# Performance work log

Hardware: AMD Instinct MI355X
Metric: run time of the kernel (lower is better)

Reference implementation:

```python
import jax, jax.numpy as jnp
import numpy as np
import math

B = 256        # batch
N = 262144     # n_data (memory bank size)
D = 128        # feat_dim
K = 4096       # number of negatives
MAX_NEGS = K   # K * max_hard_negatives_percentage (=1)
T = 0.07


def _l2norm(x):
    # Normalise(power=2): x / (sum(x^2, axis=1))^(1/2)
    return x / jnp.sqrt(jnp.sum(x * x, axis=1, keepdims=True))


def setup_inputs() -> dict:
    key = jax.random.key(0)
    k1, k2, k3, k4 = jax.random.split(key, 4)
    stdv = math.sqrt(3.0 / D)  # 1/sqrt(feat_dim/3)
    anchor_feature = _l2norm(jax.random.normal(k1, (B, D), dtype=jnp.float32))
    pair_feature = _l2norm(jax.random.normal(k2, (B, D), dtype=jnp.float32))
    memory_bank = jax.random.uniform(k3, (N, D), dtype=jnp.float32,
                                     minval=-stdv, maxval=stdv)
    membank_idx = jax.random.randint(k4, (B,), 0, N, dtype=jnp.int32)
    threshold = jnp.full((1,), 10.0, dtype=jnp.float32)  # no masking -> all-hard path
    return {"anchor_feature": anchor_feature, "pair_feature": pair_feature,
            "memory_bank": memory_bank, "membank_idx": membank_idx,
            "threshold": threshold}


def reference(anchor_feature, pair_feature, memory_bank, membank_idx, threshold):
    # ---- mine_negative_examples (no_grad in original) ----
    # NOTE: original does memory_bank.view(feat_dim, -1) == row-major reshape,
    # NOT a transpose. Replicate exactly.
    mem_r = memory_bank.reshape(D, N)                    # [D, N]
    scores = anchor_feature @ mem_r                      # [B, N]
    scores = jnp.where(scores >= threshold[0], jnp.float32(-2.0), scores)
    top_s, top_i = jax.lax.top_k(scores, K)              # [B, K]
    hard = jnp.minimum(jnp.sum(top_s != -2.0, axis=1), MAX_NEGS)  # [B]
    # random fill for positions beyond the hard count (uniform over bank;
    # original excludes a handful of indices via multinomial - negligible for large N)
    rand_i = jax.random.randint(jax.random.key(42), (B, K), 0, N, dtype=top_i.dtype)
    use_hard = jnp.arange(K)[None, :] < hard[:, None]    # [B, K]
    negatives = jnp.where(use_hard, top_i, rand_i)       # [B, K]

    # ---- contrast ----
    weight = jax.lax.stop_gradient(memory_bank[negatives])          # [B, K, D]
    weight = jnp.concatenate([pair_feature[:, None, :], weight], 1)  # slot 0 = positive, [B, K+1, D]
    out = jnp.exp(jnp.einsum('bkd,bd->bk', weight, anchor_feature) / T)  # [B, K+1]
    # params[2] == -1 initially -> Z_c = out.mean() * n_data (a detached scalar)
    Z = jax.lax.stop_gradient(jnp.mean(out) * N)
    return (out / Z)[:, :, None]                         # [B, K+1, 1]
```

## Files before the change

### kernel.cpp

```cpp
#include <hip/hip_runtime.h>
#include <math.h>

#define BB 256
#define NN 262144
#define DD 128
#define KK 4096
#define CAP 8192
#define NOUT (BB * (KK + 1))
#define THETA0 0.172f

#define RB 16
#define CB 1024
#define NRBLK (BB / RB)
#define NCSL (NN / CB)
#define SLOTS 56
#define PAD 32
#define SMEMS ((2 * 4 * CB) * 4 + RB * SLOTS * 8 + 3 * RB * 4)

typedef float f16v __attribute__((ext_vector_type(16)));

__global__ __launch_bounds__(256) void k_init(const float* __restrict__ anchor,
                                              float* __restrict__ At2,
                                              unsigned* __restrict__ cnt) {
  const int b = blockIdx.x;
  if (b < NRBLK) {
    for (int j = threadIdx.x; j < DD * 16; j += 256) {
      const int d = j >> 4, r = j & 15;
      At2[(size_t)b * DD * 16 + j] =
          anchor[(size_t)(b * RB + r) * DD + d];
    }
  } else {
    for (int i = threadIdx.x; i < BB * PAD; i += 256) cnt[i] = 0u;
  }
}

#define LOADA2(VA, VB, PTR, OFF0, OFF1)                                  \
  asm volatile("s_load_dwordx16 %0, %2, " OFF0 "\n\t"                    \
               "s_load_dwordx16 %1, %2, " OFF1 "\n\t"                    \
               "s_waitcnt lgkmcnt(0)"                                    \
               : "=&s"(VA), "=&s"(VB)                                    \
               : "s"(PTR));                                              \
  __builtin_amdgcn_sched_barrier(0);

__global__ __launch_bounds__(256, 4) void k_score(
    const float* __restrict__ bank, const float* __restrict__ At2,
    const float* __restrict__ thr, unsigned* __restrict__ cnt,
    unsigned long long* __restrict__ cand) {
  extern __shared__ float smem[];
  float* Bs = smem;
  unsigned long long* stash = (unsigned long long*)(smem + 2 * 4 * CB);
  unsigned* lcnt  = (unsigned*)(stash + RB * SLOTS);
  unsigned* lbase = lcnt + RB;
  unsigned* lm    = lbase + RB;

  const int tid = threadIdx.x;
  const int wave = tid >> 6;
  const int lane = tid & 63;
  const int bid = blockIdx.x;
  const int xcd = bid & 7;
  const int u = bid >> 3;
  const int rowblk = u & (NRBLK - 1);
  const int sgrp = u >> 4;
  const int rowbase = rowblk * RB;
  const int cb = (sgrp * 8 + xcd) * CB;

  const float* __restrict__ abase = At2 + (size_t)rowblk * DD * 16;

#define STAGE(SLOT, D0)                                                      \
  for (int t = wave; t < 16; t += 4) {                                       \
    const int d_ = t >> 2, q_ = t & 3;                                       \
    const float* gsrc =                                                      \
        bank + (size_t)((D0) + d_) * NN + cb + q_ * 256 + lane * 4;          \
    __builtin_amdgcn_global_load_lds(                                        \
        (const __attribute__((address_space(1))) void*)gsrc,                 \
        (__attribute__((address_space(3))) void*)                            \
            &Bs[((size_t)(SLOT)*4 + d_) * CB + q_ * 256],                    \
        16, 0, 0);                                                           \
  }

  STAGE(0, 0)
  STAGE(1, 4)

  const float tv = thr[0];

  float acc[64];
#pragma unroll
  for (int i = 0; i < 64; ++i) acc[i] = 0.f;

#define COMP_D(AV, DDI)                                                  \
  {                                                                      \
    const float4 bv = *(const float4*)&Bc[(DDI) * CB + 4 * tid];         \
    _Pragma("unroll") for (int r = 0; r < 16; ++r) {                     \
      acc[r * 4 + 0] = fmaf(AV[r], bv.x, acc[r * 4 + 0]);                \
      acc[r * 4 + 1] = fmaf(AV[r], bv.y, acc[r * 4 + 1]);                \
      acc[r * 4 + 2] = fmaf(AV[r], bv.z, acc[r * 4 + 2]);                \
      acc[r * 4 + 3] = fmaf(AV[r], bv.w, acc[r * 4 + 3]);                \
    }                                                                    \
  }

  for (int ch = 0; ch < 32; ++ch) {
    const float* __restrict__ Bc = &Bs[(size_t)(ch & 1) * 4 * CB];
    const float* pc = abase + ch * 64;

    if (ch < 31) { asm volatile("s_waitcnt vmcnt(4)" ::: "memory"); }
    else         { asm volatile("s_waitcnt vmcnt(0)" ::: "memory"); }
    __builtin_amdgcn_sched_barrier(0);

    f16v aA, aB, aC, aD;
    LOADA2(aA, aB, pc, "0x0", "0x40")
    COMP_D(aA, 0)
    COMP_D(aB, 1)
    LOADA2(aC, aD, pc, "0x80", "0xc0")
    COMP_D(aC, 2)
    COMP_D(aD, 3)

    if (ch < 30) {
      asm volatile("s_waitcnt lgkmcnt(0)" ::: "memory");
      __builtin_amdgcn_sched_barrier(0);
      STAGE(ch & 1, (ch + 2) * 4)
    }
  }
#undef COMP_D
#undef STAGE

  if (tid < RB) lcnt[tid] = 0u;
  __syncthreads();

#pragma unroll
  for (int r = 0; r < RB; ++r) {
#pragma unroll
    for (int c = 0; c < 4; ++c) {
      const float s = acc[r * 4 + c];
      if (s >= THETA0 && s < tv) {
        const unsigned col = (unsigned)(cb + tid * 4 + c);
        const unsigned long long key =
            ((unsigned long long)__float_as_uint(s) << 32) |
            (unsigned long long)(0xFFFFFFFFu - col);
        const unsigned lpos = atomicAdd(&lcnt[r], 1u);
        if (lpos < SLOTS) {
          stash[r * SLOTS + lpos] = key;
        } else {
          const unsigned gpos = atomicAdd(&cnt[(size_t)(rowbase + r) * PAD], 1u);
          if (gpos < CAP) cand[(size_t)(rowbase + r) * CAP + gpos] = key;
        }
      }
    }
  }
  __syncthreads();

  if (tid < RB) {
    const unsigned m = min(lcnt[tid], (unsigned)SLOTS);
    lm[tid] = m;
    lbase[tid] = atomicAdd(&cnt[(size_t)(rowbase + tid) * PAD], m);
  }
  __syncthreads();

  for (int i = tid; i < RB * SLOTS; i += 256) {
    const int r = i / SLOTS, j = i - r * SLOTS;
    if ((unsigned)j < lm[r]) {
      const unsigned pos = lbase[r] + (unsigned)j;
      if (pos < CAP) cand[(size_t)(rowbase + r) * CAP + pos] = stash[i];
    }
  }
}

__global__ void k_sort(const unsigned* __restrict__ cnt,
                       const unsigned long long* __restrict__ cand,
                       unsigned* __restrict__ neg) {
  extern __shared__ unsigned long long sk[];
  const int b = blockIdx.x;
  unsigned m = cnt[(size_t)b * PAD];
  if (m > CAP) m = CAP;

  for (int i = threadIdx.x; i < CAP; i += (int)blockDim.x)
    sk[i] = (i < (int)m) ? cand[(size_t)b * CAP + i] : 0ULL;
  __syncthreads();

  for (int k = 2; k <= CAP; k <<= 1) {
    for (int j = k >> 1; j > 0; j >>= 1) {
      for (int i = threadIdx.x; i < CAP / 2; i += (int)blockDim.x) {
        int t = i & (j - 1);
        int p = ((i - t) << 1) + t;
        int q = p + j;
        bool up = ((p & k) == 0);
        unsigned long long a = sk[p], c = sk[q];
        bool sw = up ? (a < c) : (a > c);
        if (sw) { sk[p] = c; sk[q] = a; }
      }
      __syncthreads();
    }
  }

  for (int i = threadIdx.x; i < KK; i += (int)blockDim.x) {
    unsigned idx = 0xFFFFFFFFu - (unsigned)(sk[i] & 0xFFFFFFFFull);
    neg[(size_t)b * KK + i] = (sk[i] == 0ULL) ? 0u : idx;
  }
}

__global__ __launch_bounds__(256) void k_contrast(
    const float* __restrict__ anchor, const float* __restrict__ pair,
    const float* __restrict__ bank, const unsigned* __restrict__ neg,
    float* __restrict__ out, double* __restrict__ zpart) {
  __shared__ __align__(16) float As[DD];
  __shared__ double wsum[4];
  const int bid = blockIdx.x;
  double myv;
  if (bid < BB * (KK / 256)) {
    const int b = bid >> 4;
    const int k = ((bid & 15) << 8) + threadIdx.x;
    if (threadIdx.x < DD) As[threadIdx.x] = anchor[(size_t)b * DD + threadIdx.x];
    __syncthreads();
    const unsigned idx = neg[(size_t)b * KK + k];
    const float4* __restrict__ rp = (const float4*)(bank + (size_t)idx * DD);
    const float4* __restrict__ apv = (const float4*)As;
    float s = 0.f;
#pragma unroll
    for (int q = 0; q < DD / 4; ++q) {
      float4 rv = rp[q], av = apv[q];
      s = fmaf(rv.x, av.x, s);
      s = fmaf(rv.y, av.y, s);
      s = fmaf(rv.z, av.z, s);
      s = fmaf(rv.w, av.w, s);
    }
    float e = expf(s * (1.0f / 0.07f));
    out[(size_t)b * (KK + 1) + 1 + k] = e;
    myv = (double)e;
  } else {
    const int b = threadIdx.x;
    const float* __restrict__ apr = anchor + (size_t)b * DD;
    const float* __restrict__ ppr = pair + (size_t)b * DD;
    float s = 0.f;
#pragma unroll
    for (int q = 0; q < DD; ++q) s = fmaf(apr[q], ppr[q], s);
    float e = expf(s * (1.0f / 0.07f));
    out[(size_t)b * (KK + 1)] = e;
    myv = (double)e;
  }
  for (int off = 32; off > 0; off >>= 1) myv += __shfl_down(myv, off, 64);
  if ((threadIdx.x & 63) == 0) wsum[threadIdx.x >> 6] = myv;
  __syncthreads();
  if (threadIdx.x == 0) zpart[bid] = (wsum[0] + wsum[1]) + (wsum[2] + wsum[3]);
}

__global__ void k_zreduce(const double* __restrict__ zpart, double* __restrict__ invZ) {
  __shared__ double w[16];
  double v = 0.0;
  for (int i = threadIdx.x; i < BB * (KK / 256) + 1; i += 1024) v += zpart[i];
  for (int off = 32; off > 0; off >>= 1) v += __shfl_down(v, off, 64);
  if ((threadIdx.x & 63) == 0) w[threadIdx.x >> 6] = v;
  __syncthreads();
  if (threadIdx.x == 0) {
    double t = 0.0;
    for (int q = 0; q < 16; ++q) t += w[q];
    double Z = t / ((double)BB * (double)(KK + 1)) * (double)NN;
    invZ[0] = 1.0 / Z;
  }
}

__global__ void k_scale(float* __restrict__ out, const double* __restrict__ invZ) {
  double iz = invZ[0];
  int i = blockIdx.x * 512 + threadIdx.x;
  if (i < NOUT) out[i] = (float)((double)out[i] * iz);
}

extern "C" void kernel_launch(void* const* d_in, const int* in_sizes, int n_in,
                              void* d_out, int out_size, void* d_ws, size_t ws_size,
                              hipStream_t stream) {
  const float* anchor = (const float*)d_in[0];
  const float* pair   = (const float*)d_in[1];
  const float* bank   = (const float*)d_in[2];
  const float* thr    = (const float*)d_in[4];
  float* out = (float*)d_out;

  char* w = (char*)d_ws;
  unsigned* cnt = (unsigned*)(w);
  unsigned long long* cand = (unsigned long long*)(w + BB * PAD * 4);
  unsigned* neg = (unsigned*)(w + BB * PAD * 4 + (size_t)BB * CAP * 8);
  double* zpart = (double*)(w + BB * PAD * 4 + (size_t)BB * CAP * 8 + (size_t)BB * KK * 4);
  double* invZ  = (double*)((char*)zpart + (size_t)(BB * (KK / 256) + 1) * 8);
  float*  At2   = (float*)((char*)invZ + 256);

  k_init<<<NRBLK + 1, 256, 0, stream>>>(anchor, At2, cnt);
  (void)hipFuncSetAttribute((const void*)k_score,
                            hipFuncAttributeMaxDynamicSharedMemorySize, SMEMS);
  k_score<<<NRBLK * NCSL, 256, SMEMS, stream>>>(bank, At2, thr, cnt, cand);
  (void)hipFuncSetAttribute((const void*)k_sort,
                            hipFuncAttributeMaxDynamicSharedMemorySize, CAP * 8);
  k_sort<<<BB, 1024, CAP * 8, stream>>>(cnt, cand, neg);
  k_contrast<<<BB * (KK / 256) + 1, 256, 0, stream>>>(anchor, pair, bank, neg, out, zpart);
  k_zreduce<<<1, 1024, 0, stream>>>(zpart, invZ);
  k_scale<<<(NOUT + 511) / 512, 512, 0, stream>>>(out, invZ);
}
```

Measured before the change: 392.6 us.

## Rewrite bitonic sort with register-resident elements and wave shuffles

Each thread of the per-row bitonic sort now holds 8 keys in registers. Compare-exchange stages with small strides run inside the thread's registers, mid strides use 64-lane xor shuffles, and only strides of 512 or more go through shared memory with barriers. This removes most __syncthreads and LDS traffic from the sort's many stages. The kernel now assumes a 1024-thread launch and a 64-wide wavefront, and it uses more registers per thread.

Measured after the change: 423.8 us. +7.9%, slower.

```diff
diff --git a/kernel.cpp b/kernel.cpp
--- a/kernel.cpp
+++ b/kernel.cpp
@@ -164,36 +164,70 @@
   }
 }
 
-__global__ void k_sort(const unsigned* __restrict__ cnt,
-                       const unsigned long long* __restrict__ cand,
-                       unsigned* __restrict__ neg) {
+__global__ __launch_bounds__(1024) void k_sort(
+    const unsigned* __restrict__ cnt,
+    const unsigned long long* __restrict__ cand,
+    unsigned* __restrict__ neg) {
   extern __shared__ unsigned long long sk[];
   const int b = blockIdx.x;
+  const int t = threadIdx.x;
   unsigned m = cnt[(size_t)b * PAD];
   if (m > CAP) m = CAP;
 
-  for (int i = threadIdx.x; i < CAP; i += (int)blockDim.x)
-    sk[i] = (i < (int)m) ? cand[(size_t)b * CAP + i] : 0ULL;
-  __syncthreads();
+  unsigned long long e[8];
+#pragma unroll
+  for (int s = 0; s < 8; ++s) {
+    const int i = t * 8 + s;
+    e[s] = (i < (int)m) ? cand[(size_t)b * CAP + i] : 0ULL;
+  }
 
   for (int k = 2; k <= CAP; k <<= 1) {
     for (int j = k >> 1; j > 0; j >>= 1) {
-      for (int i = threadIdx.x; i < CAP / 2; i += (int)blockDim.x) {
-        int t = i & (j - 1);
-        int p = ((i - t) << 1) + t;
-        int q = p + j;
-        bool up = ((p & k) == 0);
-        unsigned long long a = sk[p], c = sk[q];
-        bool sw = up ? (a < c) : (a > c);
-        if (sw) { sk[p] = c; sk[q] = a; }
+      if (j >= 512) {
+#pragma unroll
+        for (int s = 0; s < 8; ++s) sk[t * 8 + s] = e[s];
+        __syncthreads();
+#pragma unroll
+        for (int s = 0; s < 8; ++s) {
+          const int i = t * 8 + s;
+          const unsigned long long v = sk[i ^ j];
+          const bool keepmax = ((i & k) == 0) == ((i & j) == 0);
+          e[s] = keepmax ? (e[s] > v ? e[s] : v) : (e[s] > v ? v : e[s]);
+        }
+        __syncthreads();
+      } else if (j >= 8) {
+        const int d = j >> 3;
+#pragma unroll
+        for (int s = 0; s < 8; ++s) {
+          const unsigned long long v = __shfl_xor(e[s], d, 64);
+          const int i = t * 8 + s;
+          const bool keepmax = ((i & k) == 0) == ((i & j) == 0);
+          e[s] = keepmax ? (e[s] > v ? e[s] : v) : (e[s] > v ? v : e[s]);
+        }
+      } else {
+#pragma unroll
+        for (int s = 0; s < 8; ++s) {
+          if ((s & j) == 0) {
+            const int s2 = s | j;
+            const int i = t * 8 + s;
+            const bool up = ((i & k) == 0);
+            const unsigned long long a = e[s], c2 = e[s2];
+            const bool sw = up ? (a < c2) : (a > c2);
+            if (sw) { e[s] = c2; e[s2] = a; }
+          }
+        }
       }
-      __syncthreads();
-    }
-  }
-
-  for (int i = threadIdx.x; i < KK; i += (int)blockDim.x) {
-    unsigned idx = 0xFFFFFFFFu - (unsigned)(sk[i] & 0xFFFFFFFFull);
-    neg[(size_t)b * KK + i] = (sk[i] == 0ULL) ? 0u : idx;
+    }
+  }
+
+  if (t < KK / 8) {
+#pragma unroll
+    for (int s = 0; s < 8; ++s) {
+      const int i = t * 8 + s;
+      const unsigned long long key = e[s];
+      const unsigned idx = 0xFFFFFFFFu - (unsigned)(key & 0xFFFFFFFFull);
+      neg[(size_t)b * KK + i] = (key == 0ULL) ? 0u : idx;
+    }
   }
 }
 
```
